# Kernel tuning notes

Measured on AMD Instinct MI355X. Metric: run time of the kernel, lower is better.

## Reference

```python
import jax, jax.numpy as jnp
import numpy as np

S, B, H = 1024, 8, 1024   # seq (num_tokens//WORLD_SIZE), batch, hidden
T = S * B                 # total tokens
E, K, F = 8, 2, 4096      # experts, top_k, ffn hidden (4*H)


def setup_inputs() -> dict:
    key = jax.random.key(0)
    k0, k1, k2, k3, k4 = jax.random.split(key, 5)
    hidden_states = jax.random.normal(k0, (S, B, H), dtype=jnp.float32)
    # precomputed top-k router probs (normalized like softmax top-k output)
    gw = jax.random.uniform(k1, (T, K), dtype=jnp.float32) + 1e-3
    gate_weight = gw / jnp.sum(gw, axis=-1, keepdims=True)
    choosed_experts = jax.random.randint(k2, (T, K), 0, E).astype(jnp.int64)
    w1 = jax.random.normal(k3, (E, H, F), dtype=jnp.float32) * 0.02
    w2 = jax.random.normal(k4, (E, F, H), dtype=jnp.float32) * 0.02
    return {"hidden_states": hidden_states, "gate_weight": gate_weight,
            "choosed_experts": choosed_experts, "w1": w1, "w2": w2}


def reference(hidden_states, gate_weight, choosed_experts, w1, w2):
    # Megatron MoE with precomputed routing: dispatch tokens to top-k experts,
    # per-expert MLP (fc1 -> gelu -> fc2, no bias), combine weighted by probs.
    x = hidden_states.reshape(-1, H)  # [T, H]
    n_exp = w1.shape[0]
    # coef[t, e] = sum_k gate_weight[t, k] * 1[choosed_experts[t, k] == e]
    onehot = jax.nn.one_hot(choosed_experts, n_exp, dtype=gate_weight.dtype)  # [T, K, E]
    coef = jnp.einsum('tk,tke->te', gate_weight, onehot)  # [T, E]
    out = jnp.zeros_like(x)
    for e in range(n_exp):  # fixed small loop over experts (grouped GEMM)
        h = jax.nn.gelu(x @ w1[e])          # [T, F]
        out = out + coef[:, e:e + 1] * (h @ w2[e])  # [T, H]
    output = out.reshape(-1, H)
    return output  # mlp_bias is None in grouped-GEMM Megatron experts
```

## Files before the change

kernel.cpp:

```cpp
#include <hip/hip_runtime.h>
#include <stdint.h>

#define T 8192
#define H 1024
#define F 4096
#define E 8
#define K_TOP 2
#define TK (T * K_TOP)

#define BM 128
#define BN 128
#define BK 32

typedef unsigned short u16;
typedef __bf16 bf16x8 __attribute__((ext_vector_type(8)));
typedef float f32x4 __attribute__((ext_vector_type(4)));

__device__ __forceinline__ u16 f2bf(float f) {
    union { float f; uint32_t u; } v; v.f = f;
    uint32_t r = v.u + 0x7FFFu + ((v.u >> 16) & 1u);
    return (u16)(r >> 16);
}

__device__ __forceinline__ void async_cp16(const u16* g, u16* l) {
    __builtin_amdgcn_global_load_lds(
        (const __attribute__((address_space(1))) void*)g,
        (__attribute__((address_space(3))) void*)l, 16, 0, 0);
}

__global__ __launch_bounds__(256) void count_kernel(const int* __restrict__ ce,
                                                    int* __restrict__ counts) {
    int p = blockIdx.x * 256 + threadIdx.x;
    if (p < TK) atomicAdd(&counts[ce[p]], 1);
}

__global__ void scan_kernel(const int* __restrict__ counts, int* __restrict__ offsets) {
    if (threadIdx.x == 0) {
        int s = 0;
        for (int e = 0; e < E; e++) { offsets[e] = s; s += counts[e]; }
    }
}

__global__ __launch_bounds__(256) void fill_kernel(const int* __restrict__ ce,
                                                   const float* __restrict__ gate,
                                                   const int* __restrict__ offsets,
                                                   int* __restrict__ fill,
                                                   int* __restrict__ tokbuf,
                                                   float* __restrict__ gwbuf) {
    int p = blockIdx.x * 256 + threadIdx.x;
    if (p < TK) {
        int e = ce[p];
        int pos = offsets[e] + atomicAdd(&fill[e], 1);
        tokbuf[pos] = p >> 1;
        gwbuf[pos] = gate[p];
    }
}

__global__ __launch_bounds__(256) void cvt_bf16(const float* __restrict__ in,
                                                u16* __restrict__ out, int n) {
    int i = (blockIdx.x * 256 + threadIdx.x) * 4;
    if (i < n) {
        float4 v = *(const float4*)(in + i);
        ushort4 o;
        o.x = f2bf(v.x); o.y = f2bf(v.y); o.z = f2bf(v.z); o.w = f2bf(v.w);
        *(ushort4*)(out + i) = o;
    }
}

__global__ __launch_bounds__(256) void transpose_cvt(const float* __restrict__ in,
                                                     u16* __restrict__ out,
                                                     int R, int C) {
    __shared__ u16 tile[64][66];
    int e = blockIdx.z;
    const float* src = in + (size_t)e * R * C;
    u16* dst = out + (size_t)e * R * C;
    int c0 = blockIdx.x * 64, r0 = blockIdx.y * 64;
    int q = threadIdx.x & 15;
    int s = threadIdx.x >> 4;
#pragma unroll
    for (int p = 0; p < 4; p++) {
        int row = s + p * 16;
        float4 v = *(const float4*)(src + (size_t)(r0 + row) * C + c0 + q * 4);
        tile[row][q * 4 + 0] = f2bf(v.x);
        tile[row][q * 4 + 1] = f2bf(v.y);
        tile[row][q * 4 + 2] = f2bf(v.z);
        tile[row][q * 4 + 3] = f2bf(v.w);
    }
    __syncthreads();
#pragma unroll
    for (int p = 0; p < 4; p++) {
        int c = s + p * 16;
        ushort4 o;
        o.x = tile[q * 4 + 0][c];
        o.y = tile[q * 4 + 1][c];
        o.z = tile[q * 4 + 2][c];
        o.w = tile[q * 4 + 3][c];
        *(ushort4*)(dst + (size_t)(c0 + c) * R + r0 + q * 4) = o;
    }
}

__global__ __launch_bounds__(256, 2) void fc1_kernel(const u16* __restrict__ xb,
                                                     const u16* __restrict__ w1t,
                                                     const int* __restrict__ tokbuf,
                                                     const int* __restrict__ counts,
                                                     const int* __restrict__ offsets,
                                                     u16* __restrict__ hbuf) {
    __shared__ __align__(16) u16 As[BM * BK];
    __shared__ __align__(16) u16 Bs[BN * BK];

    const int e = blockIdx.z;
    const int cnt = counts[e];
    const int off = offsets[e];
    const int fhw = blockIdx.x + 32 * blockIdx.y;
    const int f   = (fhw & 7) * 64 + (fhw >> 3);
    const int nt  = f & 31;
    const int by  = f >> 5;

    const int tid = threadIdx.x;
    const int lane = tid & 63;
    const int wave = tid >> 6;
    const int wr = wave >> 1, wc = wave & 1;
    const int quad = lane >> 4, l16 = lane & 15;
    const int r0 = tid >> 2;
    const int kc = tid & 3;

    for (int rt = by; rt * BM < cnt; rt += 16) {
        int m0 = rt * BM + r0, m1 = m0 + 64;
        int t0 = tokbuf[off + (m0 < cnt ? m0 : cnt - 1)];
        int t1 = tokbuf[off + (m1 < cnt ? m1 : cnt - 1)];
        const u16* a0 = xb + (size_t)t0 * H + kc * 8;
        const u16* a1 = xb + (size_t)t1 * H + kc * 8;
        const u16* b0 = w1t + ((size_t)e * F + nt * BN + r0) * H + kc * 8;
        const u16* b1 = b0 + (size_t)64 * H;

        f32x4 acc[4][4];
#pragma unroll
        for (int i = 0; i < 4; i++)
#pragma unroll
            for (int j = 0; j < 4; j++) acc[i][j] = (f32x4)0.f;

        for (int k0 = 0; k0 < H; k0 += BK) {
            __syncthreads();
            async_cp16(a0 + k0, &As[tid * 8]);
            async_cp16(a1 + k0, &As[(tid + 256) * 8]);
            async_cp16(b0 + k0, &Bs[tid * 8]);
            async_cp16(b1 + k0, &Bs[(tid + 256) * 8]);
            __syncthreads();

            bf16x8 af[4], bfv[4];
#pragma unroll
            for (int mi = 0; mi < 4; mi++)
                af[mi] = *(const bf16x8*)&As[(wr * 64 + mi * 16 + l16) * BK + quad * 8];
#pragma unroll
            for (int ni = 0; ni < 4; ni++)
                bfv[ni] = *(const bf16x8*)&Bs[(wc * 64 + ni * 16 + l16) * BK + quad * 8];
#pragma unroll
            for (int mi = 0; mi < 4; mi++)
#pragma unroll
                for (int ni = 0; ni < 4; ni++)
                    acc[mi][ni] = __builtin_amdgcn_mfma_f32_16x16x32_bf16(
                        af[mi], bfv[ni], acc[mi][ni], 0, 0, 0);
        }

#pragma unroll
        for (int mi = 0; mi < 4; mi++) {
#pragma unroll
            for (int r = 0; r < 4; r++) {
                int m = rt * BM + wr * 64 + mi * 16 + quad * 4 + r;
                if (m < cnt) {
                    size_t rowbase = (size_t)(off + m) * F;
#pragma unroll
                    for (int ni = 0; ni < 4; ni++) {
                        float v = acc[mi][ni][r];
                        float u = 0.7978845608028654f * (v + 0.044715f * v * v * v);
                        float g = v / (1.f + __expf(-2.f * u));
                        int fcol = nt * BN + wc * 64 + ni * 16 + l16;
                        hbuf[rowbase + fcol] = f2bf(g);
                    }
                }
            }
        }
    }
}

__global__ __launch_bounds__(256, 2) void fc2_kernel(const u16* __restrict__ hbuf,
                                                     const u16* __restrict__ w2t,
                                                     const int* __restrict__ tokbuf,
                                                     const float* __restrict__ gwbuf,
                                                     const int* __restrict__ counts,
                                                     const int* __restrict__ offsets,
                                                     float* __restrict__ out) {
    __shared__ __align__(16) u16 As[BM * BK];
    __shared__ __align__(16) u16 Bs[BN * BK];

    const int e = blockIdx.z;
    const int cnt = counts[e];
    const int off = offsets[e];
    const int fhw = blockIdx.x + 8 * blockIdx.y;
    const int f   = (fhw & 7) * 16 + (fhw >> 3);
    const int nt  = f & 7;
    const int by  = f >> 3;

    const int tid = threadIdx.x;
    const int lane = tid & 63;
    const int wave = tid >> 6;
    const int wr = wave >> 1, wc = wave & 1;
    const int quad = lane >> 4, l16 = lane & 15;
    const int r0 = tid >> 2;
    const int kc = tid & 3;

    for (int rt = by; rt * BM < cnt; rt += 16) {
        int m0 = rt * BM + r0, m1 = m0 + 64;
        int s0 = off + (m0 < cnt ? m0 : cnt - 1);
        int s1 = off + (m1 < cnt ? m1 : cnt - 1);
        const u16* a0 = hbuf + (size_t)s0 * F + kc * 8;
        const u16* a1 = hbuf + (size_t)s1 * F + kc * 8;
        const u16* b0 = w2t + ((size_t)e * H + nt * BN + r0) * F + kc * 8;
        const u16* b1 = b0 + (size_t)64 * F;

        f32x4 acc[4][4];
#pragma unroll
        for (int i = 0; i < 4; i++)
#pragma unroll
            for (int j = 0; j < 4; j++) acc[i][j] = (f32x4)0.f;

        for (int k0 = 0; k0 < F; k0 += BK) {
            __syncthreads();
            async_cp16(a0 + k0, &As[tid * 8]);
            async_cp16(a1 + k0, &As[(tid + 256) * 8]);
            async_cp16(b0 + k0, &Bs[tid * 8]);
            async_cp16(b1 + k0, &Bs[(tid + 256) * 8]);
            __syncthreads();

            bf16x8 af[4], bfv[4];
#pragma unroll
            for (int mi = 0; mi < 4; mi++)
                af[mi] = *(const bf16x8*)&As[(wr * 64 + mi * 16 + l16) * BK + quad * 8];
#pragma unroll
            for (int ni = 0; ni < 4; ni++)
                bfv[ni] = *(const bf16x8*)&Bs[(wc * 64 + ni * 16 + l16) * BK + quad * 8];
#pragma unroll
            for (int mi = 0; mi < 4; mi++)
#pragma unroll
                for (int ni = 0; ni < 4; ni++)
                    acc[mi][ni] = __builtin_amdgcn_mfma_f32_16x16x32_bf16(
                        af[mi], bfv[ni], acc[mi][ni], 0, 0, 0);
        }

#pragma unroll
        for (int mi = 0; mi < 4; mi++) {
#pragma unroll
            for (int r = 0; r < 4; r++) {
                int m = rt * BM + wr * 64 + mi * 16 + quad * 4 + r;
                if (m < cnt) {
                    int t = tokbuf[off + m];
                    float g = gwbuf[off + m];
                    size_t obase = (size_t)t * H;
#pragma unroll
                    for (int ni = 0; ni < 4; ni++) {
                        int col = nt * BN + wc * 64 + ni * 16 + l16;
                        atomicAdd(&out[obase + col], g * acc[mi][ni][r]);
                    }
                }
            }
        }
    }
}

extern "C" void kernel_launch(void* const* d_in, const int* in_sizes, int n_in,
                              void* d_out, int out_size, void* d_ws, size_t ws_size,
                              hipStream_t stream) {
    const float* x    = (const float*)d_in[0];
    const float* gate = (const float*)d_in[1];
    const int*   ce   = (const int*)d_in[2];
    const float* w1   = (const float*)d_in[3];
    const float* w2   = (const float*)d_in[4];
    float* out = (float*)d_out;
    char* ws = (char*)d_ws;

    int*   counts  = (int*)(ws + 0);
    int*   fill    = (int*)(ws + 32);
    int*   offsets = (int*)(ws + 64);
    int*   tokbuf  = (int*)(ws + 256);
    float* gwbuf   = (float*)(ws + 256 + TK * 4);
    size_t o = 256 + (size_t)TK * 8;
    u16* xb  = (u16*)(ws + o);  o += (size_t)T * H * 2;
    u16* w1t = (u16*)(ws + o);  o += (size_t)E * F * H * 2;
    u16* w2t = (u16*)(ws + o);  o += (size_t)E * H * F * 2;
    u16* hbuf = (u16*)(ws + o);

    hipMemsetAsync(ws, 0, 256, stream);
    hipMemsetAsync(d_out, 0, (size_t)T * H * sizeof(float), stream);

    count_kernel<<<TK / 256, 256, 0, stream>>>(ce, counts);
    scan_kernel<<<1, 64, 0, stream>>>(counts, offsets);
    fill_kernel<<<TK / 256, 256, 0, stream>>>(ce, gate, offsets, fill, tokbuf, gwbuf);

    cvt_bf16<<<(T * H) / (256 * 4), 256, 0, stream>>>(x, xb, T * H);
    transpose_cvt<<<dim3(F / 64, H / 64, E), 256, 0, stream>>>(w1, w1t, H, F);
    transpose_cvt<<<dim3(H / 64, F / 64, E), 256, 0, stream>>>(w2, w2t, F, H);

    fc1_kernel<<<dim3(F / BN, 16, E), 256, 0, stream>>>(xb, w1t, tokbuf, counts, offsets, hbuf);
    fc2_kernel<<<dim3(H / BN, 16, E), 256, 0, stream>>>(hbuf, w2t, tokbuf, gwbuf, counts, offsets, out);
}
```

Before: 976.8 us.

## Double BK to 64 with XOR-swizzled LDS layout in both expert GEMMs

Raises the K-tile from 32 to 64 in the fc1 and fc2 grouped GEMM kernels, which halves the number of sync/load iterations along K. Each thread now issues four async 16-byte copies per operand instead of two. The LDS column chunk is XOR-swizzled by row, and the fragment reads apply the matching swizzle, to avoid bank conflicts on the wider rows. LDS use doubles to 32KB per block, which may limit occupancy alongside the 2-blocks-per-CU launch bound.

Result: faster. 947.5 us (-3.0%).

```diff
diff --git a/kernel.cpp b/kernel.cpp
--- a/kernel.cpp
+++ b/kernel.cpp
@@ -10,7 +10,8 @@
 
 #define BM 128
 #define BN 128
-#define BK 32
+#define BK 64
+#define TILEU (BM * BK)
 
 typedef unsigned short u16;
 typedef __bf16 bf16x8 __attribute__((ext_vector_type(8)));
@@ -105,8 +106,8 @@
                                                      const int* __restrict__ counts,
                                                      const int* __restrict__ offsets,
                                                      u16* __restrict__ hbuf) {
-    __shared__ __align__(16) u16 As[BM * BK];
-    __shared__ __align__(16) u16 Bs[BN * BK];
+    __shared__ __align__(16) u16 As[TILEU];
+    __shared__ __align__(16) u16 Bs[TILEU];
 
     const int e = blockIdx.z;
     const int cnt = counts[e];
@@ -121,17 +122,20 @@
     const int wave = tid >> 6;
     const int wr = wave >> 1, wc = wave & 1;
     const int quad = lane >> 4, l16 = lane & 15;
-    const int r0 = tid >> 2;
-    const int kc = tid & 3;
+    const int sw = l16 & 7;
+    const int rbase = tid >> 3;
+    const int kcs = ((tid & 7) ^ (rbase & 7)) * 8;
 
     for (int rt = by; rt * BM < cnt; rt += 16) {
-        int m0 = rt * BM + r0, m1 = m0 + 64;
-        int t0 = tokbuf[off + (m0 < cnt ? m0 : cnt - 1)];
-        int t1 = tokbuf[off + (m1 < cnt ? m1 : cnt - 1)];
-        const u16* a0 = xb + (size_t)t0 * H + kc * 8;
-        const u16* a1 = xb + (size_t)t1 * H + kc * 8;
-        const u16* b0 = w1t + ((size_t)e * F + nt * BN + r0) * H + kc * 8;
-        const u16* b1 = b0 + (size_t)64 * H;
+        const u16* ap[4];
+        const u16* bp[4];
+#pragma unroll
+        for (int i = 0; i < 4; i++) {
+            int m = rt * BM + rbase + 32 * i;
+            int t = tokbuf[off + (m < cnt ? m : cnt - 1)];
+            ap[i] = xb + (size_t)t * H + kcs;
+            bp[i] = w1t + ((size_t)e * F + nt * BN + rbase + 32 * i) * H + kcs;
+        }
 
         f32x4 acc[4][4];
 #pragma unroll
@@ -141,25 +145,31 @@
 
         for (int k0 = 0; k0 < H; k0 += BK) {
             __syncthreads();
-            async_cp16(a0 + k0, &As[tid * 8]);
-            async_cp16(a1 + k0, &As[(tid + 256) * 8]);
-            async_cp16(b0 + k0, &Bs[tid * 8]);
-            async_cp16(b1 + k0, &Bs[(tid + 256) * 8]);
+#pragma unroll
+            for (int i = 0; i < 4; i++) {
+                async_cp16(ap[i] + k0, &As[tid * 8 + i * 2048]);
+                async_cp16(bp[i] + k0, &Bs[tid * 8 + i * 2048]);
+            }
             __syncthreads();
 
-            bf16x8 af[4], bfv[4];
-#pragma unroll
-            for (int mi = 0; mi < 4; mi++)
-                af[mi] = *(const bf16x8*)&As[(wr * 64 + mi * 16 + l16) * BK + quad * 8];
-#pragma unroll
-            for (int ni = 0; ni < 4; ni++)
-                bfv[ni] = *(const bf16x8*)&Bs[(wc * 64 + ni * 16 + l16) * BK + quad * 8];
-#pragma unroll
-            for (int mi = 0; mi < 4; mi++)
+#pragma unroll
+            for (int ks = 0; ks < 2; ks++) {
+                bf16x8 af[4], bfv[4];
+#pragma unroll
+                for (int mi = 0; mi < 4; mi++)
+                    af[mi] = *(const bf16x8*)&As[(wr * 64 + mi * 16 + l16) * BK
+                                                 + (((ks * 4 + quad) ^ sw) * 8)];
 #pragma unroll
                 for (int ni = 0; ni < 4; ni++)
-                    acc[mi][ni] = __builtin_amdgcn_mfma_f32_16x16x32_bf16(
-                        af[mi], bfv[ni], acc[mi][ni], 0, 0, 0);
+                    bfv[ni] = *(const bf16x8*)&Bs[(wc * 64 + ni * 16 + l16) * BK
+                                                  + (((ks * 4 + quad) ^ sw) * 8)];
+#pragma unroll
+                for (int mi = 0; mi < 4; mi++)
+#pragma unroll
+                    for (int ni = 0; ni < 4; ni++)
+                        acc[mi][ni] = __builtin_amdgcn_mfma_f32_16x16x32_bf16(
+                            af[mi], bfv[ni], acc[mi][ni], 0, 0, 0);
+            }
         }
 
 #pragma unroll
@@ -190,8 +200,8 @@
                                                      const int* __restrict__ counts,
                                                      const int* __restrict__ offsets,
                                                      float* __restrict__ out) {
-    __shared__ __align__(16) u16 As[BM * BK];
-    __shared__ __align__(16) u16 Bs[BN * BK];
+    __shared__ __align__(16) u16 As[TILEU];
+    __shared__ __align__(16) u16 Bs[TILEU];
 
     const int e = blockIdx.z;
     const int cnt = counts[e];
@@ -206,17 +216,20 @@
     const int wave = tid >> 6;
     const int wr = wave >> 1, wc = wave & 1;
     const int quad = lane >> 4, l16 = lane & 15;
-    const int r0 = tid >> 2;
-    const int kc = tid & 3;
+    const int sw = l16 & 7;
+    const int rbase = tid >> 3;
+    const int kcs = ((tid & 7) ^ (rbase & 7)) * 8;
 
     for (int rt = by; rt * BM < cnt; rt += 16) {
-        int m0 = rt * BM + r0, m1 = m0 + 64;
-        int s0 = off + (m0 < cnt ? m0 : cnt - 1);
-        int s1 = off + (m1 < cnt ? m1 : cnt - 1);
-        const u16* a0 = hbuf + (size_t)s0 * F + kc * 8;
-        const u16* a1 = hbuf + (size_t)s1 * F + kc * 8;
-        const u16* b0 = w2t + ((size_t)e * H + nt * BN + r0) * F + kc * 8;
-        const u16* b1 = b0 + (size_t)64 * F;
+        const u16* ap[4];
+        const u16* bp[4];
+#pragma unroll
+        for (int i = 0; i < 4; i++) {
+            int m = rt * BM + rbase + 32 * i;
+            int s = off + (m < cnt ? m : cnt - 1);
+            ap[i] = hbuf + (size_t)s * F + kcs;
+            bp[i] = w2t + ((size_t)e * H + nt * BN + rbase + 32 * i) * F + kcs;
+        }
 
         f32x4 acc[4][4];
 #pragma unroll
@@ -226,25 +239,31 @@
 
         for (int k0 = 0; k0 < F; k0 += BK) {
             __syncthreads();
-            async_cp16(a0 + k0, &As[tid * 8]);
-            async_cp16(a1 + k0, &As[(tid + 256) * 8]);
-            async_cp16(b0 + k0, &Bs[tid * 8]);
-            async_cp16(b1 + k0, &Bs[(tid + 256) * 8]);
+#pragma unroll
+            for (int i = 0; i < 4; i++) {
+                async_cp16(ap[i] + k0, &As[tid * 8 + i * 2048]);
+                async_cp16(bp[i] + k0, &Bs[tid * 8 + i * 2048]);
+            }
             __syncthreads();
 
-            bf16x8 af[4], bfv[4];
-#pragma unroll
-            for (int mi = 0; mi < 4; mi++)
-                af[mi] = *(const bf16x8*)&As[(wr * 64 + mi * 16 + l16) * BK + quad * 8];
-#pragma unroll
-            for (int ni = 0; ni < 4; ni++)
-                bfv[ni] = *(const bf16x8*)&Bs[(wc * 64 + ni * 16 + l16) * BK + quad * 8];
-#pragma unroll
-            for (int mi = 0; mi < 4; mi++)
+#pragma unroll
+            for (int ks = 0; ks < 2; ks++) {
+                bf16x8 af[4], bfv[4];
+#pragma unroll
+                for (int mi = 0; mi < 4; mi++)
+                    af[mi] = *(const bf16x8*)&As[(wr * 64 + mi * 16 + l16) * BK
+                                                 + (((ks * 4 + quad) ^ sw) * 8)];
 #pragma unroll
                 for (int ni = 0; ni < 4; ni++)
-                    acc[mi][ni] = __builtin_amdgcn_mfma_f32_16x16x32_bf16(
-                        af[mi], bfv[ni], acc[mi][ni], 0, 0, 0);
+                    bfv[ni] = *(const bf16x8*)&Bs[(wc * 64 + ni * 16 + l16) * BK
+                                                  + (((ks * 4 + quad) ^ sw) * 8)];
+#pragma unroll
+                for (int mi = 0; mi < 4; mi++)
+#pragma unroll
+                    for (int ni = 0; ni < 4; ni++)
+                        acc[mi][ni] = __builtin_amdgcn_mfma_f32_16x16x32_bf16(
+                            af[mi], bfv[ni], acc[mi][ni], 0, 0, 0);
+            }
         }
 
 #pragma unroll
```
